# Kernel tuning notes

Hardware: AMD Instinct MI355X
Metric: run time of the kernel (lower is better)

The kernel has to match this reference:

```python
import jax, jax.numpy as jnp
import numpy as np

T, HID = 2048, 2048
H, KV, D = 16, 2, 256
ROT = 64  # head_dim * partial_rotary_factor (0.25)
THETA = 1.0e7
EPS = 1e-6
SCALE = D ** -0.5


def setup_inputs() -> dict:
    key = jax.random.key(0)
    ks = jax.random.split(key, 6)
    return {
        "positions": jnp.arange(T, dtype=jnp.int64 if jax.config.jax_enable_x64 else jnp.int32),
        "hidden_states": jax.random.normal(ks[0], (T, HID), jnp.float32),
        "wq": jax.random.normal(ks[1], (H * D * 2, HID), jnp.float32) * 0.02,
        "wk": jax.random.normal(ks[2], (KV * D, HID), jnp.float32) * 0.02,
        "wv": jax.random.normal(ks[3], (KV * D, HID), jnp.float32) * 0.02,
        "wo": jax.random.normal(ks[4], (HID, H * D), jnp.float32) * 0.02,
        "q_norm_w": jnp.zeros((D,), jnp.float32),
        "k_norm_w": jnp.zeros((D,), jnp.float32),
    }


def _rmsnorm(x, w):
    xf = x.astype(jnp.float32)
    out = xf * jax.lax.rsqrt(jnp.mean(xf * xf, axis=-1, keepdims=True) + EPS)
    return (out * (1.0 + w.astype(jnp.float32))).astype(x.dtype)


def _rope(positions, x):
    # partial rotary: first ROT dims, neox (rotate-half) style
    inv_freq = 1.0 / (THETA ** (jnp.arange(0, ROT, 2, dtype=jnp.float32) / ROT))
    freqs = positions.astype(jnp.float32)[:, None] * inv_freq  # [T, ROT/2]
    cos = jnp.cos(freqs)[:, None, :]  # [T,1,ROT/2]
    sin = jnp.sin(freqs)[:, None, :]
    x1 = x[..., : ROT // 2]
    x2 = x[..., ROT // 2 : ROT]
    rot = jnp.concatenate([x1 * cos - x2 * sin, x2 * cos + x1 * sin], axis=-1)
    return jnp.concatenate([rot, x[..., ROT:]], axis=-1)


def reference(positions, hidden_states, wq, wk, wv, wo, q_norm_w, k_norm_w):
    t = hidden_states.shape[0]
    q_out = (hidden_states @ wq.T).reshape(t, H, 2 * D)
    query, gate = q_out[..., :D], q_out[..., D:]
    gate = gate.reshape(t, H * D)
    k = (hidden_states @ wk.T).reshape(t, KV, D)
    v = (hidden_states @ wv.T).reshape(t, KV, D)

    query = _rmsnorm(query, q_norm_w)
    k = _rmsnorm(k, k_norm_w)
    query = _rope(positions, query)
    k = _rope(positions, k)

    # GQA: expand KV heads to H heads
    rep = H // KV
    k = jnp.repeat(k, rep, axis=1)  # [t, H, D]
    v = jnp.repeat(v, rep, axis=1)

    scores = jnp.einsum("qhd,khd->hqk", query, k) * SCALE
    causal = jnp.tril(jnp.ones((t, t), dtype=bool))
    scores = jnp.where(causal[None], scores, jnp.finfo(scores.dtype).min)
    probs = jax.nn.softmax(scores, axis=-1)
    o = jnp.einsum("hqk,khd->qhd", probs, v).reshape(t, H * D)

    o = o * jax.nn.sigmoid(gate)
    return o @ wo.T
```

## Files before the change

### kernel.cpp

```cpp
#include <hip/hip_runtime.h>
#include <hip/hip_bf16.h>

#define T_LEN 2048
#define HID_DIM 2048
#define NH 16
#define NKV 2
#define HD 256
#define ROT 64
#define EPS_F 1e-6f
#define SCALE_F 0.0625f
#define THETA_F 10000000.0f

typedef __bf16 bf16x8 __attribute__((ext_vector_type(8)));
typedef float floatx4 __attribute__((ext_vector_type(4)));

__device__ __forceinline__ unsigned short f2bf(float x) {
  unsigned int u = __float_as_uint(x);
  unsigned int rounding = 0x7FFFu + ((u >> 16) & 1u);
  return (unsigned short)((u + rounding) >> 16);
}
__device__ __forceinline__ float bf2f(unsigned short u) {
  return __uint_as_float(((unsigned int)u) << 16);
}
__device__ __forceinline__ floatx4 mfma16(bf16x8 a, bf16x8 b, floatx4 c) {
  return __builtin_amdgcn_mfma_f32_16x16x32_bf16(a, b, c, 0, 0, 0);
}
__device__ __forceinline__ void gl_lds16(const unsigned short* g, unsigned short* l) {
  __builtin_amdgcn_global_load_lds(
      (const __attribute__((address_space(1))) unsigned int*)g,
      (__attribute__((address_space(3))) unsigned int*)l, 16, 0, 0);
}

__global__ __launch_bounds__(256) void cvt_all(
    const float* __restrict__ hs, const float* __restrict__ wq,
    const float* __restrict__ wk, const float* __restrict__ wv,
    const float* __restrict__ wo, unsigned short* __restrict__ hsb,
    unsigned short* __restrict__ qkvwb, unsigned short* __restrict__ wob) {
  int i = blockIdx.x * 256 + threadIdx.x;
  const float4* s4;
  ushort4* d4;
  int j;
  if (i < 1048576) { s4 = (const float4*)hs; d4 = (ushort4*)hsb; j = i; }
  else if (i < 5242880) { s4 = (const float4*)wq; d4 = (ushort4*)qkvwb; j = i - 1048576; }
  else if (i < 5505024) { s4 = (const float4*)wk; d4 = (ushort4*)qkvwb + 4194304; j = i - 5242880; }
  else if (i < 5767168) { s4 = (const float4*)wv; d4 = (ushort4*)qkvwb + 4456448; j = i - 5505024; }
  else { s4 = (const float4*)wo; d4 = (ushort4*)wob; j = i - 5767168; }
  float4 v = s4[j];
  ushort4 o;
  o.x = f2bf(v.x); o.y = f2bf(v.y); o.z = f2bf(v.z); o.w = f2bf(v.w);
  d4[j] = o;
}

__global__ __launch_bounds__(256) void gemm_bf16_bt(
    const unsigned short* __restrict__ A,
    const unsigned short* __restrict__ B,
    void* __restrict__ Cv, int M, int N, int ld, int Ksub, int c_bf16,
    unsigned short* __restrict__ vTout) {
  __shared__ alignas(16) unsigned short As[2][128 * 32];
  __shared__ alignas(16) unsigned short Bs[2][128 * 32];
  const int tid = threadIdx.x;
  const int m0 = blockIdx.y * 128;
  const int n0 = blockIdx.x * 128;
  const int koff = blockIdx.z * Ksub;
  const int lane = tid & 63;
  const int wave = tid >> 6;
  const int wm = (wave >> 1) * 64;
  const int wn = (wave & 1) * 64;
  const int lrow = lane & 15;
  const int kgrp = lane >> 4;

  const unsigned short* aG = A + (size_t)(m0 + wave * 32 + (lane >> 2)) * ld + (lane & 3) * 8 + koff;
  const unsigned short* bG = B + (size_t)(n0 + wave * 32 + (lane >> 2)) * ld + (lane & 3) * 8 + koff;

  auto stage = [&](int k0, int b) {
    gl_lds16(aG + k0, &As[b][(wave * 32) * 32]);
    gl_lds16(aG + (size_t)16 * ld + k0, &As[b][(wave * 32 + 16) * 32]);
    gl_lds16(bG + k0, &Bs[b][(wave * 32) * 32]);
    gl_lds16(bG + (size_t)16 * ld + k0, &Bs[b][(wave * 32 + 16) * 32]);
  };

  floatx4 acc[4][4];
#pragma unroll
  for (int i = 0; i < 4; i++)
#pragma unroll
    for (int j = 0; j < 4; j++) acc[i][j] = floatx4{0.f, 0.f, 0.f, 0.f};

  stage(0, 0);
  __syncthreads();
  int cur = 0;
  for (int k0 = 0; k0 < Ksub; k0 += 32) {
    if (k0 + 32 < Ksub) stage(k0 + 32, cur ^ 1);
    bf16x8 af[4], bfr[4];
#pragma unroll
    for (int i = 0; i < 4; i++)
      af[i] = *reinterpret_cast<const bf16x8*>(&As[cur][(wm + i * 16 + lrow) * 32 + kgrp * 8]);
#pragma unroll
    for (int j = 0; j < 4; j++)
      bfr[j] = *reinterpret_cast<const bf16x8*>(&Bs[cur][(wn + j * 16 + lrow) * 32 + kgrp * 8]);
#pragma unroll
    for (int i = 0; i < 4; i++)
#pragma unroll
      for (int j = 0; j < 4; j++)
        acc[i][j] = mfma16(af[i], bfr[j], acc[i][j]);
    __syncthreads();
    cur ^= 1;
  }

  if (c_bf16) {
    unsigned short* C = (unsigned short*)Cv;
    const bool vtile = (vTout != nullptr) && (n0 >= 8704);
#pragma unroll
    for (int i = 0; i < 4; i++) {
      int row = m0 + wm + i * 16 + kgrp * 4;
#pragma unroll
      for (int j = 0; j < 4; j++) {
        int col = n0 + wn + j * 16 + lrow;
        if (vtile) {
          unsigned short* vrow = vTout + (size_t)(col - 8704) * T_LEN + row;
#pragma unroll
          for (int r = 0; r < 4; r++) vrow[r] = f2bf(acc[i][j][r]);
        } else {
#pragma unroll
          for (int r = 0; r < 4; r++)
            C[(size_t)(row + r) * N + col] = f2bf(acc[i][j][r]);
        }
      }
    }
  } else {
    float* C = (float*)Cv + (size_t)blockIdx.z * M * N;
#pragma unroll
    for (int i = 0; i < 4; i++) {
      int row = m0 + wm + i * 16 + kgrp * 4;
#pragma unroll
      for (int j = 0; j < 4; j++) {
        int col = n0 + wn + j * 16 + lrow;
#pragma unroll
        for (int r = 0; r < 4; r++)
          C[(size_t)(row + r) * N + col] = acc[i][j][r];
      }
    }
  }
}

__global__ __launch_bounds__(256) void add_out(
    const float* __restrict__ p, float* __restrict__ out, int n4) {
  int i = blockIdx.x * 256 + threadIdx.x;
  if (i >= n4) return;
  float4 a = ((const float4*)p)[i];
  float4 b = ((const float4*)p)[i + n4];
  float4 o;
  o.x = a.x + b.x; o.y = a.y + b.y; o.z = a.z + b.z; o.w = a.w + b.w;
  ((float4*)out)[i] = o;
}

__global__ __launch_bounds__(256) void norm_rope(
    const unsigned short* __restrict__ in, const float* __restrict__ w,
    const int* __restrict__ pos, unsigned short* __restrict__ outb,
    int in_rs, int in_hs, int out_rs) {
  const int t = blockIdx.x, h = blockIdx.y, d = threadIdx.x;
  float x = bf2f(in[(size_t)t * in_rs + h * in_hs + d]);
  float ss = x * x;
#pragma unroll
  for (int m = 32; m >= 1; m >>= 1) ss += __shfl_xor(ss, m);
  __shared__ float wsum[4];
  if ((d & 63) == 0) wsum[d >> 6] = ss;
  __syncthreads();
  float tot = (wsum[0] + wsum[1]) + (wsum[2] + wsum[3]);
  float rms = rsqrtf(tot * (1.0f / 256.0f) + EPS_F);
  float y = x * rms * (1.0f + w[d]);
  float o = y;
  if (d < ROT) {
    float partner = __shfl_xor(y, ROT / 2);
    int i = d & (ROT / 2 - 1);
    float fr = (float)pos[t] * exp2f(-(float)i * (23.2534966642f / 32.0f));
    float c = cosf(fr), s = sinf(fr);
    o = (d < ROT / 2) ? (y * c - partner * s) : (partner * s + y * c);
  }
  outb[(size_t)t * out_rs + h * HD + d] = f2bf(o);
}

__global__ __launch_bounds__(256, 2) void attn_fwd(
    const unsigned short* __restrict__ qbf,
    const unsigned short* __restrict__ kbf,
    const unsigned short* __restrict__ vT,
    const unsigned short* __restrict__ qkvout,
    unsigned short* __restrict__ og)
{
  const int t = 31 - (int)blockIdx.x;
  const int h = blockIdx.y;
  const int wv = threadIdx.x >> 6;
  const int lane = threadIdx.x & 63;
  const int lrow = lane & 15;
  const int kgrp = lane >> 4;
  const int kv = h >> 3;
  const int q0 = t * 64 + wv * 16;
  const int nb = t * 2 + 2;

  __shared__ alignas(16) unsigned short Ks[32 * 256];
  __shared__ alignas(16) unsigned short Vs[2][256 * 32];
  __shared__ alignas(16) unsigned short Ps[4][16 * 32];

  auto stage_k = [&](int kb) {
#pragma unroll
    for (int i = 0; i < 4; ++i) {
      const int inst = wv * 4 + i;
      const int key_loc = inst * 2 + (lane >> 5);
      const int c = (lane & 31) ^ (key_loc & 7);
      const unsigned short* g =
          kbf + (size_t)(kb + key_loc) * (NKV * HD) + kv * HD + c * 8;
      gl_lds16(g, &Ks[inst * 512]);
    }
  };
  auto stage_v = [&](int kb, int buf) {
#pragma unroll
    for (int i = 0; i < 4; ++i) {
      const int inst = wv * 4 + i;
      const int dim = inst * 16 + (lane >> 2);
      const int c = (lane & 3) ^ (dim & 3);
      const unsigned short* g =
          vT + (size_t)(kv * HD + dim) * T_LEN + kb + c * 8;
      gl_lds16(g, &Vs[buf][inst * 512]);
    }
  };

  bf16x8 qa[8];
  {
    const unsigned short* qr = qbf + (size_t)(q0 + lrow) * (NH * HD) + h * HD + kgrp * 8;
#pragma unroll
    for (int s = 0; s < 8; s++)
      qa[s] = *reinterpret_cast<const bf16x8*>(qr + s * 32);
  }

  float lp[4] = {0.f, 0.f, 0.f, 0.f};
  floatx4 o[16];
#pragma unroll
  for (int dt = 0; dt < 16; dt++) o[dt] = floatx4{0.f, 0.f, 0.f, 0.f};

  stage_k(0);
  stage_v(0, 0);

  for (int ib = 0; ib < nb; ++ib) {
    const int kb = ib * 32;
    __syncthreads();
    if (ib + 1 < nb) stage_v(kb + 32, (ib + 1) & 1);

    const bool d = kb <= q0 + 15;

    floatx4 s0[2];
#pragma unroll
    for (int j = 0; j < 2; j++) s0[j] = floatx4{0.f, 0.f, 0.f, 0.f};
#pragma unroll
    for (int j = 0; j < 2; ++j) {
      const int ks = kb + j * 16;
      if (!(d && (ks <= q0 + 15))) continue;
      bf16x8 kf[8];
#pragma unroll
      for (int s = 0; s < 8; s++)
        kf[s] = *reinterpret_cast<const bf16x8*>(
            &Ks[(j * 16 + lrow) * 256 + (((s * 4 + kgrp) ^ (lrow & 7)) * 8)]);
#pragma unroll
      for (int s = 0; s < 8; s++) s0[j] = mfma16(qa[s], kf[s], s0[j]);
    }

    if (d) {
#pragma unroll
      for (int r = 0; r < 4; ++r) {
        const int qr = q0 + kgrp * 4 + r;
        float p0 = (kb + lrow <= qr) ? __expf(s0[0][r] * SCALE_F) : 0.f;
        float p1 = (kb + 16 + lrow <= qr) ? __expf(s0[1][r] * SCALE_F) : 0.f;
        lp[r] += p0 + p1;
        Ps[wv][(kgrp * 4 + r) * 32 + lrow] = f2bf(p0);
        Ps[wv][(kgrp * 4 + r) * 32 + 16 + lrow] = f2bf(p1);
      }
    }

    __syncthreads();
    if (ib + 1 < nb) stage_k(kb + 32);

    if (d) {
      bf16x8 pa = *reinterpret_cast<const bf16x8*>(&Ps[wv][lrow * 32 + kgrp * 8]);
      const unsigned short* vsb = &Vs[ib & 1][0];
#pragma unroll
      for (int dt = 0; dt < 16; ++dt) {
        const int dd = dt * 16 + lrow;
        bf16x8 bv = *reinterpret_cast<const bf16x8*>(
            &vsb[dd * 32 + ((kgrp ^ (lrow & 3)) * 8)]);
        o[dt] = mfma16(pa, bv, o[dt]);
      }
    }
  }

#pragma unroll
  for (int r = 0; r < 4; ++r) {
#pragma unroll
    for (int m = 8; m >= 1; m >>= 1) lp[r] += __shfl_xor(lp[r], m);
  }

#pragma unroll
  for (int r = 0; r < 4; ++r) {
    const int row = q0 + kgrp * 4 + r;
    const float inv_l = 1.0f / lp[r];
    const unsigned short* grow = qkvout + (size_t)row * 9216 + h * 512 + 256;
    unsigned short* orow = og + (size_t)row * (NH * HD) + h * HD;
#pragma unroll
    for (int dt = 0; dt < 16; dt++) {
      int dim = dt * 16 + lrow;
      float g = bf2f(grow[dim]);
      float val = o[dt][r] * inv_l;
      val *= 1.0f / (1.0f + __expf(-g));
      orow[dim] = f2bf(val);
    }
  }
}

extern "C" void kernel_launch(void* const* d_in, const int* in_sizes, int n_in,
                              void* d_out, int out_size, void* d_ws, size_t ws_size,
                              hipStream_t stream) {
  const int* positions = (const int*)d_in[0];
  const float* hidden = (const float*)d_in[1];
  const float* wq = (const float*)d_in[2];
  const float* wk = (const float*)d_in[3];
  const float* wv = (const float*)d_in[4];
  const float* wo = (const float*)d_in[5];
  const float* qnw = (const float*)d_in[6];
  const float* knw = (const float*)d_in[7];
  float* out = (float*)d_out;

  char* ws = (char*)d_ws;
  size_t off = 0;
  auto alloc = [&](size_t elems) -> unsigned short* {
    unsigned short* p = (unsigned short*)(ws + off);
    off += (elems * 2 + 255) & ~(size_t)255;
    return p;
  };
  unsigned short* hsb    = alloc((size_t)T_LEN * HID_DIM);
  unsigned short* qkvwb  = alloc((size_t)9216 * HID_DIM);
  unsigned short* wob    = alloc((size_t)HID_DIM * NH * HD);
  unsigned short* qkvout = alloc((size_t)T_LEN * 9216);
  unsigned short* qbf    = alloc((size_t)T_LEN * NH * HD);
  unsigned short* kbf    = alloc((size_t)T_LEN * NKV * HD);
  unsigned short* vTb    = alloc((size_t)NKV * HD * T_LEN);
  unsigned short* og     = alloc((size_t)T_LEN * NH * HD);
  float* part = (float*)ws;

  cvt_all<<<30720, 256, 0, stream>>>(hidden, wq, wk, wv, wo, hsb, qkvwb, wob);

  gemm_bf16_bt<<<dim3(72, 16, 1), 256, 0, stream>>>(hsb, qkvwb, qkvout, 2048, 9216, 2048, 2048, 1, vTb);

  norm_rope<<<dim3(T_LEN, NH), 256, 0, stream>>>(qkvout, qnw, positions, qbf, 9216, 512, NH * HD);
  norm_rope<<<dim3(T_LEN, NKV), 256, 0, stream>>>(qkvout + 8192, knw, positions, kbf, 9216, HD, NKV * HD);

  attn_fwd<<<dim3(32, NH), 256, 0, stream>>>(qbf, kbf, vTb, qkvout, og);

  gemm_bf16_bt<<<dim3(16, 16, 2), 256, 0, stream>>>(og, wob, part, 2048, 2048, 4096, 2048, 0, nullptr);
  add_out<<<4096, 256, 0, stream>>>(part, out, 1048576);
}
```

Before: 443.7 us.

## Fuse Q/K norm-rope into one vectorized launch and add MFMA priority hints

Replaces the two per-head norm_rope launches with one kernel in which each wavefront handles a whole head, using 4-element vector loads and stores and a wave-only reduction with no shared memory or block barrier. Q and K heads share a single grid, which removes one launch and cuts the block count. In the attention kernel, MFMA loops are wrapped in s_setprio raises, and a __syncthreads is replaced by a raw s_barrier between sched_barrier fences to steer instruction scheduling. Risks: the K-branch blocks idle two of their four waves, and the raw barrier depends on LDS ordering still being correct without the implicit waitcnt that __syncthreads would emit.

New measurement: 456.0 us. +2.8%, slower.

```diff
diff --git a/kernel.cpp b/kernel.cpp
--- a/kernel.cpp
+++ b/kernel.cpp
@@ -153,30 +153,64 @@
   ((float4*)out)[i] = o;
 }
 
-__global__ __launch_bounds__(256) void norm_rope(
-    const unsigned short* __restrict__ in, const float* __restrict__ w,
-    const int* __restrict__ pos, unsigned short* __restrict__ outb,
-    int in_rs, int in_hs, int out_rs) {
-  const int t = blockIdx.x, h = blockIdx.y, d = threadIdx.x;
-  float x = bf2f(in[(size_t)t * in_rs + h * in_hs + d]);
-  float ss = x * x;
+__global__ __launch_bounds__(256) void norm_rope_fused(
+    const unsigned short* __restrict__ qkv, const float* __restrict__ qw,
+    const float* __restrict__ kw, const int* __restrict__ pos,
+    unsigned short* __restrict__ qbf, unsigned short* __restrict__ kbf) {
+  const int t = blockIdx.x;
+  const int y = blockIdx.y;
+  const int wv = threadIdx.x >> 6;
+  const int lane = threadIdx.x & 63;
+  const unsigned short* in;
+  const float* w;
+  unsigned short* outp;
+  if (y < 4) {
+    const int h = y * 4 + wv;
+    in = qkv + (size_t)t * 9216 + h * 512;
+    w = qw;
+    outp = qbf + (size_t)t * (NH * HD) + h * HD;
+  } else {
+    if (wv >= NKV) return;
+    in = qkv + (size_t)t * 9216 + 8192 + wv * HD;
+    w = kw;
+    outp = kbf + (size_t)t * (NKV * HD) + wv * HD;
+  }
+  const int d0 = lane * 4;
+  ushort4 v = *reinterpret_cast<const ushort4*>(in + d0);
+  float x0 = bf2f(v.x), x1 = bf2f(v.y), x2 = bf2f(v.z), x3 = bf2f(v.w);
+  float ss = (x0 * x0 + x1 * x1) + (x2 * x2 + x3 * x3);
 #pragma unroll
   for (int m = 32; m >= 1; m >>= 1) ss += __shfl_xor(ss, m);
-  __shared__ float wsum[4];
-  if ((d & 63) == 0) wsum[d >> 6] = ss;
-  __syncthreads();
-  float tot = (wsum[0] + wsum[1]) + (wsum[2] + wsum[3]);
-  float rms = rsqrtf(tot * (1.0f / 256.0f) + EPS_F);
-  float y = x * rms * (1.0f + w[d]);
-  float o = y;
-  if (d < ROT) {
-    float partner = __shfl_xor(y, ROT / 2);
-    int i = d & (ROT / 2 - 1);
-    float fr = (float)pos[t] * exp2f(-(float)i * (23.2534966642f / 32.0f));
-    float c = cosf(fr), s = sinf(fr);
-    o = (d < ROT / 2) ? (y * c - partner * s) : (partner * s + y * c);
-  }
-  outb[(size_t)t * out_rs + h * HD + d] = f2bf(o);
+  const float rms = rsqrtf(ss * (1.0f / 256.0f) + EPS_F);
+  float4 w4 = *reinterpret_cast<const float4*>(w + d0);
+  float y0 = x0 * rms * (1.0f + w4.x);
+  float y1 = x1 * rms * (1.0f + w4.y);
+  float y2 = x2 * rms * (1.0f + w4.z);
+  float y3 = x3 * rms * (1.0f + w4.w);
+  if (lane < 16) {
+    float p0 = __shfl_xor(y0, 8);
+    float p1 = __shfl_xor(y1, 8);
+    float p2 = __shfl_xor(y2, 8);
+    float p3 = __shfl_xor(y3, 8);
+    const float pp = (float)pos[t];
+    const float k = 23.2534966642f / 32.0f;
+    float o0, o1, o2, o3;
+#pragma unroll
+    for (int j = 0; j < 4; ++j) {
+      const int d = d0 + j;
+      const int i = d & 31;
+      const float fr = pp * exp2f(-(float)i * k);
+      const float c = cosf(fr), s = sinf(fr);
+      const float yj = (j == 0) ? y0 : (j == 1) ? y1 : (j == 2) ? y2 : y3;
+      const float pj = (j == 0) ? p0 : (j == 1) ? p1 : (j == 2) ? p2 : p3;
+      const float oj = (d < 32) ? (yj * c - pj * s) : (pj * s + yj * c);
+      if (j == 0) o0 = oj; else if (j == 1) o1 = oj; else if (j == 2) o2 = oj; else o3 = oj;
+    }
+    y0 = o0; y1 = o1; y2 = o2; y3 = o3;
+  }
+  ushort4 ov;
+  ov.x = f2bf(y0); ov.y = f2bf(y1); ov.z = f2bf(y2); ov.w = f2bf(y3);
+  *reinterpret_cast<ushort4*>(outp + d0) = ov;
 }
 
 __global__ __launch_bounds__(256, 2) void attn_fwd(
@@ -258,8 +292,10 @@
       for (int s = 0; s < 8; s++)
         kf[s] = *reinterpret_cast<const bf16x8*>(
             &Ks[(j * 16 + lrow) * 256 + (((s * 4 + kgrp) ^ (lrow & 7)) * 8)]);
+      __builtin_amdgcn_s_setprio(1);
 #pragma unroll
       for (int s = 0; s < 8; s++) s0[j] = mfma16(qa[s], kf[s], s0[j]);
+      __builtin_amdgcn_s_setprio(0);
     }
 
     if (d) {
@@ -274,12 +310,15 @@
       }
     }
 
-    __syncthreads();
+    __builtin_amdgcn_sched_barrier(0);
+    __builtin_amdgcn_s_barrier();
+    __builtin_amdgcn_sched_barrier(0);
     if (ib + 1 < nb) stage_k(kb + 32);
 
     if (d) {
       bf16x8 pa = *reinterpret_cast<const bf16x8*>(&Ps[wv][lrow * 32 + kgrp * 8]);
       const unsigned short* vsb = &Vs[ib & 1][0];
+      __builtin_amdgcn_s_setprio(1);
 #pragma unroll
       for (int dt = 0; dt < 16; ++dt) {
         const int dd = dt * 16 + lrow;
@@ -287,6 +326,7 @@
             &vsb[dd * 32 + ((kgrp ^ (lrow & 3)) * 8)]);
         o[dt] = mfma16(pa, bv, o[dt]);
       }
+      __builtin_amdgcn_s_setprio(0);
     }
   }
 
@@ -347,8 +387,7 @@
 
   gemm_bf16_bt<<<dim3(72, 16, 1), 256, 0, stream>>>(hsb, qkvwb, qkvout, 2048, 9216, 2048, 2048, 1, vTb);
 
-  norm_rope<<<dim3(T_LEN, NH), 256, 0, stream>>>(qkvout, qnw, positions, qbf, 9216, 512, NH * HD);
-  norm_rope<<<dim3(T_LEN, NKV), 256, 0, stream>>>(qkvout + 8192, knw, positions, kbf, 9216, HD, NKV * HD);
+  norm_rope_fused<<<dim3(T_LEN, 5), 256, 0, stream>>>(qkvout, qnw, knw, positions, qbf, kbf);
 
   attn_fwd<<<dim3(32, NH), 256, 0, stream>>>(qbf, kbf, vTb, qkvout, og);
 
```
